# Optimization experiments

Hardware: AMD Instinct MI355X
Metric: run time of the kernel (lower is better)

Reference implementation:

```python
import jax, jax.numpy as jnp
import numpy as np

N_EMBD = 1024
N_HEAD = 16
B, T = 8, 1024
EPS = 1e-5


def setup_inputs() -> dict:
    key = jax.random.key(0)
    ks = jax.random.split(key, 12)
    C = N_EMBD
    s_in = 1.0 / np.sqrt(C)
    s_ff = 1.0 / np.sqrt(4 * C)
    inp = {
        "x": jax.random.normal(ks[0], (B, T, C), dtype=jnp.float32),
        "mask": jnp.tril(jnp.ones((T, T), dtype=jnp.int32))[None, None, :, :],
        "ln1_w": jnp.ones((C,), jnp.float32),
        "ln1_b": jnp.zeros((C,), jnp.float32),
        "ln2_w": jnp.ones((C,), jnp.float32),
        "ln2_b": jnp.zeros((C,), jnp.float32),
        "wq": jax.random.normal(ks[1], (C, C), jnp.float32) * s_in,
        "bq": jnp.zeros((C,), jnp.float32),
        "wk": jax.random.normal(ks[2], (C, C), jnp.float32) * s_in,
        "bk": jnp.zeros((C,), jnp.float32),
        "wv": jax.random.normal(ks[3], (C, C), jnp.float32) * s_in,
        "bv": jnp.zeros((C,), jnp.float32),
        "wo": jax.random.normal(ks[4], (C, C), jnp.float32) * s_in,
        "bo": jnp.zeros((C,), jnp.float32),
        "w1": jax.random.normal(ks[5], (C, 4 * C), jnp.float32) * s_in,
        "b1": jnp.zeros((4 * C,), jnp.float32),
        "w2": jax.random.normal(ks[6], (4 * C, C), jnp.float32) * s_ff,
        "b2": jnp.zeros((C,), jnp.float32),
    }
    return inp


def _layer_norm(x, w, b):
    mu = jnp.mean(x, axis=-1, keepdims=True)
    var = jnp.mean(jnp.square(x - mu), axis=-1, keepdims=True)
    return (x - mu) * jax.lax.rsqrt(var + EPS) * w + b


def reference(x, mask, ln1_w, ln1_b, ln2_w, ln2_b,
              wq, bq, wk, bk, wv, bv, wo, bo, w1, b1, w2, b2):
    Bx, Tx, C = x.shape
    H = N_HEAD
    d = C // H
    h = _layer_norm(x, ln1_w, ln1_b)
    q = (h @ wq + bq).reshape(Bx, Tx, H, d)
    k = (h @ wk + bk).reshape(Bx, Tx, H, d)
    v = (h @ wv + bv).reshape(Bx, Tx, H, d)
    # [B,H,Tq,Tk] scores, scaled by sqrt(head_dim)
    scores = jnp.einsum('bqhd,bkhd->bhqk', q, k) / jnp.sqrt(jnp.float32(d))
    scores = jnp.where(mask == 0, -jnp.inf, scores)
    attn = jax.nn.softmax(scores, axis=-1)
    ctx = jnp.einsum('bhqk,bkhd->bqhd', attn, v).reshape(Bx, Tx, C)
    x = x + (ctx @ wo + bo)
    h2 = _layer_norm(x, ln2_w, ln2_b)
    ff = jax.nn.gelu(h2 @ w1 + b1, approximate=False) @ w2 + b2
    return x + ff
```

## Files before the change

### kernel.cpp

```cpp
#include <hip/hip_runtime.h>
#include <hip/hip_bf16.h>
#include <math.h>


#define DEVI __device__ __forceinline__

typedef __attribute__((ext_vector_type(4))) float floatx4;
typedef __attribute__((ext_vector_type(16))) float floatx16;
typedef __attribute__((ext_vector_type(8))) short shortx8;

DEVI ushort f2b(float f) {
    __hip_bfloat16 h = __float2bfloat16(f);
    return __builtin_bit_cast(ushort, h);
}

DEVI void gl_lds16(const ushort* g, ushort* l) {
    __builtin_amdgcn_global_load_lds(
        (const __attribute__((address_space(1))) void*)g,
        (__attribute__((address_space(3))) void*)l, 16, 0, 0);
}

DEVI float gelu_f(float v) {
    const float u0 = 0.7978845608f * v * (1.0f + 0.044715f * v * v);
    const float u  = fminf(fmaxf(u0, -15.0f), 15.0f);
    const float e  = exp2f(u * 2.885390082f);
    const float th = 1.0f - 2.0f / (e + 1.0f);
    return 0.5f * v * (1.0f + th);
}

__global__ void transp4_kernel(const float* __restrict__ s0, const float* __restrict__ s1,
                               const float* __restrict__ s2, const float* __restrict__ s3,
                               ushort* __restrict__ d0, ushort* __restrict__ d1,
                               ushort* __restrict__ d2, ushort* __restrict__ d3) {
    const int z = blockIdx.z;
    const float* src = (z == 0) ? s0 : (z == 1) ? s1 : (z == 2) ? s2 : s3;
    ushort*      dst = (z == 0) ? d0 : (z == 1) ? d1 : (z == 2) ? d2 : d3;
    __shared__ float tile[32][33];
    const int c0 = blockIdx.x * 32, r0 = blockIdx.y * 32;
    const int tx = threadIdx.x, ty = threadIdx.y;
#pragma unroll
    for (int i = 0; i < 32; i += 8)
        tile[ty + i][tx] = src[(size_t)(r0 + ty + i) * 1024 + c0 + tx];
    __syncthreads();
#pragma unroll
    for (int i = 0; i < 32; i += 8)
        dst[(size_t)(c0 + ty + i) * 1024 + r0 + tx] = f2b(tile[tx][ty + i]);
}

__global__ void transp_kernel(const float* __restrict__ src,
                              ushort* __restrict__ dst, int R, int C) {
    __shared__ float tile[32][33];
    const int c0 = blockIdx.x * 32, r0 = blockIdx.y * 32;
    const int tx = threadIdx.x, ty = threadIdx.y;
#pragma unroll
    for (int i = 0; i < 32; i += 8)
        tile[ty + i][tx] = src[(size_t)(r0 + ty + i) * C + c0 + tx];
    __syncthreads();
#pragma unroll
    for (int i = 0; i < 32; i += 8)
        dst[(size_t)(c0 + ty + i) * R + r0 + tx] = f2b(tile[tx][ty + i]);
}

__global__ __launch_bounds__(256)
void ln_kernel(const float* __restrict__ x, const float* __restrict__ w,
               const float* __restrict__ b, ushort* __restrict__ out) {
    __shared__ float red[8];
    const int m = blockIdx.x;
    const int tid = threadIdx.x;
    const float4 xv = *(const float4*)&x[(size_t)m * 1024 + tid * 4];
    float s  = xv.x + xv.y + xv.z + xv.w;
    float s2 = xv.x * xv.x + xv.y * xv.y + xv.z * xv.z + xv.w * xv.w;
#pragma unroll
    for (int o = 32; o >= 1; o >>= 1) {
        s  += __shfl_xor(s, o, 64);
        s2 += __shfl_xor(s2, o, 64);
    }
    const int wv_ = tid >> 6;
    if ((tid & 63) == 0) { red[wv_] = s; red[4 + wv_] = s2; }
    __syncthreads();
    s  = red[0] + red[1] + red[2] + red[3];
    s2 = red[4] + red[5] + red[6] + red[7];
    const float mu   = s * (1.0f / 1024.0f);
    const float var  = s2 * (1.0f / 1024.0f) - mu * mu;
    const float rstd = rsqrtf(var + 1e-5f);
    const float4 wv = *(const float4*)&w[tid * 4];
    const float4 bv = *(const float4*)&b[tid * 4];
    ushort o4[4];
    o4[0] = f2b((xv.x - mu) * rstd * wv.x + bv.x);
    o4[1] = f2b((xv.y - mu) * rstd * wv.y + bv.y);
    o4[2] = f2b((xv.z - mu) * rstd * wv.z + bv.z);
    o4[3] = f2b((xv.w - mu) * rstd * wv.w + bv.w);
    *(uint2*)&out[(size_t)m * 1024 + tid * 4] = *(uint2*)o4;
}

template <int MODE>
__global__ __launch_bounds__(256, 2)
void gemm_big(const ushort* __restrict__ A, const ushort* __restrict__ Bt,
              const float* __restrict__ biasQ, const float* __restrict__ biasK,
              const float* __restrict__ biasV,
              void* __restrict__ out, void* __restrict__ out2, void* __restrict__ out3,
              int N, int K) {
    __shared__ ushort lds[(256 + 128) * 64];
    ushort* sA = lds;
    ushort* sB = lds + 256 * 64;

    const int tid  = threadIdx.x;
    const int lane = tid & 63;
    const int wave = tid >> 6;
    const int l31  = lane & 31;
    const int half = lane >> 5;
    const int wm   = (wave & 1) * 128;
    const int wn   = (wave >> 1) * 64;
    const int m0   = blockIdx.y * 256;
    const int n0   = blockIdx.x * 128;

    floatx16 acc[4][2] = {};

    const int lrow = lane >> 3;
    const int scb  = (lane & 7) ^ lrow;
    const ushort* Ag = A  + (size_t)(m0 + wave * 8 + lrow) * K + scb * 8;
    const ushort* Bg = Bt + (size_t)(n0 + wave * 8 + lrow) * K + scb * 8;

    for (int k0 = 0; k0 < K; k0 += 64) {
        __syncthreads();
#pragma unroll
        for (int p = 0; p < 8; ++p)
            gl_lds16(Ag + (size_t)(p * 32) * K + k0, sA + (p * 32 + wave * 8) * 64);
#pragma unroll
        for (int p = 0; p < 4; ++p)
            gl_lds16(Bg + (size_t)(p * 32) * K + k0, sB + (p * 32 + wave * 8) * 64);
        __syncthreads();
#pragma unroll
        for (int ks = 0; ks < 4; ++ks) {
            const int cx = ks * 2 + half;
            shortx8 af[4], bf[2];
#pragma unroll
            for (int i = 0; i < 4; ++i) {
                const int r = wm + i * 32 + l31;
                af[i] = *(const shortx8*)&sA[r * 64 + (cx ^ (r & 7)) * 8];
            }
#pragma unroll
            for (int j = 0; j < 2; ++j) {
                const int r = wn + j * 32 + l31;
                bf[j] = *(const shortx8*)&sB[r * 64 + (cx ^ (r & 7)) * 8];
            }
#pragma unroll
            for (int i = 0; i < 4; ++i)
#pragma unroll
                for (int j = 0; j < 2; ++j)
                    acc[i][j] = __builtin_amdgcn_mfma_f32_32x32x16_bf16(
                        af[i], bf[j], acc[i][j], 0, 0, 0);
        }
    }

    if constexpr (MODE == 1) {
        const int mat = n0 >> 10;
        if (mat < 2) {
            const float* bp = (mat == 0) ? biasQ : biasK;
            ushort* dst = (mat == 0) ? (ushort*)out : (ushort*)out2;
            const int bb = m0 >> 10;
            const int tbase = m0 & 1023;
#pragma unroll
            for (int i = 0; i < 4; ++i)
#pragma unroll
                for (int j = 0; j < 2; ++j) {
                    const int cn = (n0 & 1023) + wn + j * 32 + l31;
                    const float bv = bp[cn];
                    const int h = cn >> 6, dd = cn & 63;
#pragma unroll
                    for (int reg = 0; reg < 16; ++reg) {
                        const int t = tbase + wm + i * 32 + (reg & 3) + 8 * (reg >> 2) + 4 * half;
                        dst[((size_t)(bb * 16 + h) * 1024 + t) * 64 + dd] =
                            f2b(acc[i][j][reg] + bv);
                    }
                }
        } else {
            ushort* T = lds;
            const int vb = n0 - 2048;
            const int bb = m0 >> 10;
#pragma unroll
            for (int hf = 0; hf < 2; ++hf) {
                __syncthreads();
                if ((wave & 1) == hf) {
#pragma unroll
                    for (int i = 0; i < 4; ++i)
#pragma unroll
                        for (int j = 0; j < 2; ++j) {
                            const int dim = wn + j * 32 + l31;
                            const float bv = biasV[vb + dim];
#pragma unroll
                            for (int rq = 0; rq < 4; ++rq) {
                                const int tloc = i * 32 + 8 * rq + 4 * half;
                                ushort pk[4];
#pragma unroll
                                for (int e = 0; e < 4; ++e)
                                    pk[e] = f2b(acc[i][j][rq * 4 + e] + bv);
                                *(uint2*)&T[dim * 136 + tloc] = *(uint2*)pk;
                            }
                        }
                }
                __syncthreads();
#pragma unroll
                for (int pass = 0; pass < 8; ++pass) {
                    const int row = pass * 16 + (tid >> 4);
                    const int cb  = (tid & 15) * 8;
                    const uint4 val = *(const uint4*)&T[row * 136 + cb];
                    const int dd = vb + row;
                    const int h = dd >> 6, dl = dd & 63;
                    const int t = (m0 & 1023) + hf * 128 + cb;
                    *(uint4*)&((ushort*)out3)[((size_t)(bb * 16 + h) * 64 + dl) * 1024 + t] = val;
                }
            }
        }
    } else {
#pragma unroll
        for (int i = 0; i < 4; ++i)
#pragma unroll
            for (int j = 0; j < 2; ++j) {
                const int gn = n0 + wn + j * 32 + l31;
                const float bv = biasQ[gn];
#pragma unroll
                for (int reg = 0; reg < 16; ++reg) {
                    const int gm = m0 + wm + i * 32 + (reg & 3) + 8 * (reg >> 2) + 4 * half;
                    const float v = acc[i][j][reg] + bv;
                    ((ushort*)out)[(size_t)gm * N + gn] = f2b(gelu_f(v));
                }
            }
    }
}

__global__ __launch_bounds__(256)
void gemm_res(const ushort* __restrict__ A, const ushort* __restrict__ Bt,
              const float* __restrict__ bias, float* __restrict__ out,
              const float* __restrict__ resid, int N, int K) {
    __shared__ ushort lds[128 * 64 * 2];
    ushort* sA = lds;
    ushort* sB = lds + 128 * 64;

    const int tid  = threadIdx.x;
    const int lane = tid & 63;
    const int wave = tid >> 6;
    const int l31  = lane & 31;
    const int half = lane >> 5;
    const int wm   = (wave & 1) * 64;
    const int wn   = (wave >> 1) * 64;
    const int m0   = blockIdx.y * 128;
    const int n0   = blockIdx.x * 128;

    floatx16 acc[2][2] = {};

    const int lrow = lane >> 3;
    const int scb  = (lane & 7) ^ lrow;
    const ushort* Ag = A  + (size_t)(m0 + wave * 8 + lrow) * K + scb * 8;
    const ushort* Bg = Bt + (size_t)(n0 + wave * 8 + lrow) * K + scb * 8;

    for (int k0 = 0; k0 < K; k0 += 64) {
        __syncthreads();
#pragma unroll
        for (int p = 0; p < 4; ++p) {
            gl_lds16(Ag + (size_t)(p * 32) * K + k0, sA + (p * 32 + wave * 8) * 64);
            gl_lds16(Bg + (size_t)(p * 32) * K + k0, sB + (p * 32 + wave * 8) * 64);
        }
        __syncthreads();
#pragma unroll
        for (int ks = 0; ks < 4; ++ks) {
            const int cx = ks * 2 + half;
            shortx8 af[2], bf[2];
#pragma unroll
            for (int i = 0; i < 2; ++i) {
                const int r = wm + i * 32 + l31;
                af[i] = *(const shortx8*)&sA[r * 64 + (cx ^ (r & 7)) * 8];
            }
#pragma unroll
            for (int j = 0; j < 2; ++j) {
                const int r = wn + j * 32 + l31;
                bf[j] = *(const shortx8*)&sB[r * 64 + (cx ^ (r & 7)) * 8];
            }
#pragma unroll
            for (int i = 0; i < 2; ++i)
#pragma unroll
                for (int j = 0; j < 2; ++j)
                    acc[i][j] = __builtin_amdgcn_mfma_f32_32x32x16_bf16(
                        af[i], bf[j], acc[i][j], 0, 0, 0);
        }
    }
#pragma unroll
    for (int i = 0; i < 2; ++i)
#pragma unroll
        for (int j = 0; j < 2; ++j) {
            const int gn = n0 + wn + j * 32 + l31;
            const float bv = bias[gn];
#pragma unroll
            for (int reg = 0; reg < 16; ++reg) {
                const int gm = m0 + wm + i * 32 + (reg & 3) + 8 * (reg >> 2) + 4 * half;
                out[(size_t)gm * N + gn] =
                    acc[i][j][reg] + bv + resid[(size_t)gm * N + gn];
            }
        }
}

__global__ __launch_bounds__(256)
void attn_kernel(const ushort* __restrict__ Q, const ushort* __restrict__ Kk,
                 const ushort* __restrict__ Vt, ushort* __restrict__ ctx) {
    __shared__ ushort sK[64 * 64];
    __shared__ ushort sV[64 * 64];
    __shared__ ushort sP[4][16 * 72];

    const int tid  = threadIdx.x;
    const int lane = tid & 63;
    const int wave = tid >> 6;
    const int quad = lane >> 4;
    const int l15  = lane & 15;

    const int qb = 15 - (blockIdx.x >> 7);
    const int bh = blockIdx.x & 127;
    const size_t base = (size_t)bh << 16;
    const int bb = bh >> 4, h = bh & 15;

    const int lrow = lane >> 3;
    const int scb  = (lane & 7) ^ lrow;
    const ushort* Kg = Kk + base + (size_t)(wave * 8 + lrow) * 64 + scb * 8;
    const ushort* Vg = Vt + base + (size_t)(wave * 8 + lrow) * 1024 + scb * 8;

    const int qrow = qb * 64 + wave * 16 + l15;
    const shortx8 qf0 = *(const shortx8*)&Q[base + (size_t)qrow * 64 + quad * 8];
    const shortx8 qf1 = *(const shortx8*)&Q[base + (size_t)qrow * 64 + 32 + quad * 8];

    const float SC = 0.125f * 1.44269504f;

    float mstate[4], lstate[4];
    floatx4 oacc[4] = {};
#pragma unroll
    for (int r = 0; r < 4; ++r) { mstate[r] = -__builtin_inff(); lstate[r] = 0.0f; }

    for (int kt = 0; kt <= qb; ++kt) {
        __syncthreads();
#pragma unroll
        for (int p = 0; p < 2; ++p) {
            gl_lds16(Kg + (size_t)kt * 4096 + (size_t)p * 2048,
                     sK + (p * 32 + wave * 8) * 64);
            gl_lds16(Vg + (size_t)kt * 64 + (size_t)p * 32 * 1024,
                     sV + (p * 32 + wave * 8) * 64);
        }
        __syncthreads();

        floatx4 s[4];
#pragma unroll
        for (int nt = 0; nt < 4; ++nt) {
            const int r = nt * 16 + l15;
            const int c0 = quad ^ (r & 7);
            const int c1 = (4 + quad) ^ (r & 7);
            const shortx8 kf0 = *(const shortx8*)&sK[r * 64 + c0 * 8];
            const shortx8 kf1 = *(const shortx8*)&sK[r * 64 + c1 * 8];
            floatx4 z = {};
            z = __builtin_amdgcn_mfma_f32_16x16x32_bf16(qf0, kf0, z, 0, 0, 0);
            z = __builtin_amdgcn_mfma_f32_16x16x32_bf16(qf1, kf1, z, 0, 0, 0);
            s[nt] = z;
        }
#pragma unroll
        for (int nt = 0; nt < 4; ++nt)
#pragma unroll
            for (int r = 0; r < 4; ++r) {
                float sv = s[nt][r] * SC;
                if (kt == qb) {
                    const int col = nt * 16 + l15;
                    const int row = wave * 16 + quad * 4 + r;
                    if (col > row) sv = -__builtin_inff();
                }
                s[nt][r] = sv;
            }
        float mnew[4], alpha[4];
#pragma unroll
        for (int r = 0; r < 4; ++r) {
            float mt = fmaxf(fmaxf(s[0][r], s[1][r]), fmaxf(s[2][r], s[3][r]));
#pragma unroll
            for (int o = 8; o >= 1; o >>= 1) mt = fmaxf(mt, __shfl_xor(mt, o, 64));
            mnew[r]  = fmaxf(mstate[r], mt);
            alpha[r] = exp2f(mstate[r] - mnew[r]);
            mstate[r] = mnew[r];
        }
#pragma unroll
        for (int r = 0; r < 4; ++r) {
            float rs = 0.0f;
#pragma unroll
            for (int nt = 0; nt < 4; ++nt) {
                const float p = exp2f(s[nt][r] - mnew[r]);
                s[nt][r] = p;
                rs += p;
            }
#pragma unroll
            for (int o = 8; o >= 1; o >>= 1) rs += __shfl_xor(rs, o, 64);
            lstate[r] = alpha[r] * lstate[r] + rs;
#pragma unroll
            for (int dt = 0; dt < 4; ++dt) oacc[dt][r] *= alpha[r];
        }
#pragma unroll
        for (int nt = 0; nt < 4; ++nt)
#pragma unroll
            for (int r = 0; r < 4; ++r)
                sP[wave][(quad * 4 + r) * 72 + nt * 16 + l15] = f2b(s[nt][r]);
        __asm__ volatile("s_waitcnt lgkmcnt(0)" ::: "memory");
        const shortx8 pf0 = *(const shortx8*)&sP[wave][l15 * 72 + quad * 8];
        const shortx8 pf1 = *(const shortx8*)&sP[wave][l15 * 72 + 32 + quad * 8];
#pragma unroll
        for (int dt = 0; dt < 4; ++dt) {
            const int r = dt * 16 + l15;
            const int c0 = quad ^ (r & 7);
            const int c1 = (4 + quad) ^ (r & 7);
            const shortx8 v0 = *(const shortx8*)&sV[r * 64 + c0 * 8];
            const shortx8 v1 = *(const shortx8*)&sV[r * 64 + c1 * 8];
            oacc[dt] = __builtin_amdgcn_mfma_f32_16x16x32_bf16(pf0, v0, oacc[dt], 0, 0, 0);
            oacc[dt] = __builtin_amdgcn_mfma_f32_16x16x32_bf16(pf1, v1, oacc[dt], 0, 0, 0);
        }
    }
#pragma unroll
    for (int dt = 0; dt < 4; ++dt)
#pragma unroll
        for (int r = 0; r < 4; ++r) {
            const int t = qb * 64 + wave * 16 + quad * 4 + r;
            const int dim = dt * 16 + l15;
            const float v = oacc[dt][r] / lstate[r];
            ctx[(size_t)(bb * 1024 + t) * 1024 + h * 64 + dim] = f2b(v);
        }
}

extern "C" void kernel_launch(void* const* d_in, const int* in_sizes, int n_in,
                              void* d_out, int out_size, void* d_ws, size_t ws_size,
                              hipStream_t stream) {
    const float* x    = (const float*)d_in[0];
    const float* ln1w = (const float*)d_in[2];
    const float* ln1b = (const float*)d_in[3];
    const float* ln2w = (const float*)d_in[4];
    const float* ln2b = (const float*)d_in[5];
    const float* wq   = (const float*)d_in[6];
    const float* bq   = (const float*)d_in[7];
    const float* wk   = (const float*)d_in[8];
    const float* bk   = (const float*)d_in[9];
    const float* wv   = (const float*)d_in[10];
    const float* bv   = (const float*)d_in[11];
    const float* wo   = (const float*)d_in[12];
    const float* bo   = (const float*)d_in[13];
    const float* w1   = (const float*)d_in[14];
    const float* b1   = (const float*)d_in[15];
    const float* w2   = (const float*)d_in[16];
    const float* b2   = (const float*)d_in[17];

    char* ws = (char*)d_ws;
    const size_t MB = 1024 * 1024;
    ushort* WQKVT = (ushort*)(ws + 0 * MB);
    ushort* WOT   = (ushort*)(ws + 6 * MB);
    ushort* W1T   = (ushort*)(ws + 8 * MB);
    ushort* W2T   = (ushort*)(ws + 16 * MB);
    ushort* H1    = (ushort*)(ws + 24 * MB);
    ushort* H2    = H1;
    ushort* Qb    = (ushort*)(ws + 40 * MB);
    ushort* Kb    = (ushort*)(ws + 56 * MB);
    ushort* Vbt   = (ushort*)(ws + 72 * MB);
    ushort* FF1   = (ushort*)(ws + 40 * MB);
    ushort* CTX   = (ushort*)(ws + 104 * MB);

    float* xout = (float*)d_out;

    const dim3 tb(32, 8);
    transp4_kernel<<<dim3(32, 32, 4), tb, 0, stream>>>(
        wq, wk, wv, wo,
        WQKVT, WQKVT + 1024 * 1024, WQKVT + 2048 * 1024, WOT);
    transp_kernel<<<dim3(128, 32), tb, 0, stream>>>(w1, W1T, 1024, 4096);
    transp_kernel<<<dim3(32, 128), tb, 0, stream>>>(w2, W2T, 4096, 1024);

    ln_kernel<<<8192, 256, 0, stream>>>(x, ln1w, ln1b, H1);

    gemm_big<1><<<dim3(24, 32), 256, 0, stream>>>(H1, WQKVT, bq, bk, bv,
                                                  Qb, Kb, Vbt, 3072, 1024);

    attn_kernel<<<2048, 256, 0, stream>>>(Qb, Kb, Vbt, CTX);

    gemm_res<<<dim3(8, 64), 256, 0, stream>>>(CTX, WOT, bo, xout, x, 1024, 1024);

    ln_kernel<<<8192, 256, 0, stream>>>(xout, ln2w, ln2b, H2);

    gemm_big<3><<<dim3(32, 32), 256, 0, stream>>>(H2, W1T, b1, nullptr, nullptr,
                                                  FF1, nullptr, nullptr, 4096, 1024);

    gemm_res<<<dim3(8, 64), 256, 0, stream>>>(FF1, W2T, b2, xout, xout, 1024, 4096);

    (void)in_sizes; (void)n_in; (void)out_size; (void)ws_size;
}
```

Baseline: 497.4 us.

## Replace gemm_big with 8-wave 256x256 double-buffered pipelined GEMM

Replaces the 4-wave 256x128 GEMM used for the QKV projection and FF1 with an 8-wave 256x256 tile kernel. It double-buffers LDS, issues global-to-LDS loads for the next k-tiles interleaved with four MFMA phases, and raises MFMA priority with s_setprio. It also switches to 16x16x32 MFMAs and remaps workgroups for L2 locality. The intent is to hide global load latency and raise MFMA utilisation. The cost is 128KB of LDS per block, which limits occupancy, plus more complex manual waitcnt and barrier scheduling.

```diff
diff --git a/kernel.cpp b/kernel.cpp
--- a/kernel.cpp
+++ b/kernel.cpp
@@ -93,139 +93,207 @@
     *(uint2*)&out[(size_t)m * 1024 + tid * 4] = *(uint2*)o4;
 }
 
+
+#define STAGE_A(j, h) { const int c_ = (j) & 1;                                         \
+    gl_lds16(pA + (size_t)((h) * 128) * K + (j) * 64,                                   \
+             lds + c_ * 16384 + (h) * 8192 + dOff);                                     \
+    gl_lds16(pA + (size_t)((h) * 128 + 8) * K + (j) * 64,                               \
+             lds + c_ * 16384 + (h) * 8192 + dOff + 512); }
+
+#define STAGE_B(j, h) { const int c_ = (j) & 1;                                         \
+    gl_lds16(pB + (size_t)((h) * 128) * K + (j) * 64,                                   \
+             lds + 32768 + c_ * 16384 + (h) * 8192 + dOff);                             \
+    gl_lds16(pB + (size_t)((h) * 128 + 8) * K + (j) * 64,                               \
+             lds + 32768 + c_ * 16384 + (h) * 8192 + dOff + 512); }
+
+#define LOAD_A(mq, c) { const ushort* ap = lds + (c) * 16384 + (mq) * 8192;             \
+    _Pragma("unroll") for (int mi = 0; mi < 4; ++mi) {                                  \
+        af[mi][0] = *(const shortx8*)&ap[aBase + mi * 1024];                            \
+        af[mi][1] = *(const shortx8*)&ap[(aBase ^ 32) + mi * 1024]; } }
+
+#define LOAD_B(nq, c) { const ushort* bp = lds + 32768 + (c) * 16384 + (nq) * 8192;     \
+    _Pragma("unroll") for (int ni = 0; ni < 2; ++ni) {                                  \
+        bf[ni][0] = *(const shortx8*)&bp[bBase + ni * 1024];                            \
+        bf[ni][1] = *(const shortx8*)&bp[(bBase ^ 32) + ni * 1024]; } }
+
+#define MFMA16(mq, nq) {                                                                \
+    _Pragma("unroll") for (int mi = 0; mi < 4; ++mi)                                    \
+    _Pragma("unroll") for (int ni = 0; ni < 2; ++ni)                                    \
+    _Pragma("unroll") for (int ks = 0; ks < 2; ++ks)                                    \
+        acc[mq][mi][nq][ni] = __builtin_amdgcn_mfma_f32_16x16x32_bf16(                  \
+            af[mi][ks], bf[ni][ks], acc[mq][mi][nq][ni], 0, 0, 0); }
+
+#define PH_SYNC() { __builtin_amdgcn_s_barrier();                                       \
+    asm volatile("s_waitcnt lgkmcnt(0)" ::: "memory");                                  \
+    __builtin_amdgcn_sched_barrier(0); }
+
 template <int MODE>
-__global__ __launch_bounds__(256, 2)
-void gemm_big(const ushort* __restrict__ A, const ushort* __restrict__ Bt,
-              const float* __restrict__ biasQ, const float* __restrict__ biasK,
-              const float* __restrict__ biasV,
-              void* __restrict__ out, void* __restrict__ out2, void* __restrict__ out3,
-              int N, int K) {
-    __shared__ ushort lds[(256 + 128) * 64];
-    ushort* sA = lds;
-    ushort* sB = lds + 256 * 64;
+__global__ __launch_bounds__(512, 2)
+void gemm8(const ushort* __restrict__ A, const ushort* __restrict__ Bt,
+           const float* __restrict__ biasQ, const float* __restrict__ biasK,
+           const float* __restrict__ biasV,
+           void* __restrict__ out, void* __restrict__ out2, void* __restrict__ out3,
+           int N, int K) {
+    __shared__ __align__(16) ushort lds[65536];
 
     const int tid  = threadIdx.x;
     const int lane = tid & 63;
-    const int wave = tid >> 6;
-    const int l31  = lane & 31;
-    const int half = lane >> 5;
-    const int wm   = (wave & 1) * 128;
-    const int wn   = (wave >> 1) * 64;
-    const int m0   = blockIdx.y * 256;
-    const int n0   = blockIdx.x * 128;
-
-    floatx16 acc[4][2] = {};
-
-    const int lrow = lane >> 3;
-    const int scb  = (lane & 7) ^ lrow;
-    const ushort* Ag = A  + (size_t)(m0 + wave * 8 + lrow) * K + scb * 8;
-    const ushort* Bg = Bt + (size_t)(n0 + wave * 8 + lrow) * K + scb * 8;
-
-    for (int k0 = 0; k0 < K; k0 += 64) {
-        __syncthreads();
-#pragma unroll
-        for (int p = 0; p < 8; ++p)
-            gl_lds16(Ag + (size_t)(p * 32) * K + k0, sA + (p * 32 + wave * 8) * 64);
-#pragma unroll
-        for (int p = 0; p < 4; ++p)
-            gl_lds16(Bg + (size_t)(p * 32) * K + k0, sB + (p * 32 + wave * 8) * 64);
-        __syncthreads();
-#pragma unroll
-        for (int ks = 0; ks < 4; ++ks) {
-            const int cx = ks * 2 + half;
-            shortx8 af[4], bf[2];
-#pragma unroll
-            for (int i = 0; i < 4; ++i) {
-                const int r = wm + i * 32 + l31;
-                af[i] = *(const shortx8*)&sA[r * 64 + (cx ^ (r & 7)) * 8];
-            }
-#pragma unroll
-            for (int j = 0; j < 2; ++j) {
-                const int r = wn + j * 32 + l31;
-                bf[j] = *(const shortx8*)&sB[r * 64 + (cx ^ (r & 7)) * 8];
-            }
-#pragma unroll
-            for (int i = 0; i < 4; ++i)
-#pragma unroll
-                for (int j = 0; j < 2; ++j)
-                    acc[i][j] = __builtin_amdgcn_mfma_f32_32x32x16_bf16(
-                        af[i], bf[j], acc[i][j], 0, 0, 0);
+    const int w    = tid >> 6;
+    const int wr   = w >> 2;
+    const int wc   = w & 3;
+
+    int bx = blockIdx.x, by = blockIdx.y;
+    {
+        const int nwg = gridDim.x * gridDim.y;
+        if ((nwg & 7) == 0) {
+            const int flat = by * gridDim.x + bx;
+            const int cpx  = nwg >> 3;
+            const int wg   = (flat & 7) * cpx + (flat >> 3);
+            bx = wg % gridDim.x;
+            by = wg / gridDim.x;
+        }
+    }
+    const int m0 = by * 256;
+    const int n0 = bx * 256;
+    const int NT = K >> 6;
+
+    floatx4 acc[2][4][2][2] = {};
+
+    const int lr3 = lane >> 3;
+    const int sc  = (lane & 7) ^ lr3;
+    const ushort* pA = A  + (size_t)(m0 + w * 16 + lr3) * K + sc * 8;
+    const ushort* pB = Bt + (size_t)(n0 + w * 16 + lr3) * K + sc * 8;
+    const int dOff = w * 1024;
+
+    const int c0    = (lane >> 4) ^ (lane & 7);
+    const int aBase = (wr * 64 + (lane & 15)) * 64 + c0 * 8;
+    const int bBase = (wc * 32 + (lane & 15)) * 64 + c0 * 8;
+
+    shortx8 af[4][2], bf[2][2];
+
+    STAGE_A(0, 0); STAGE_B(0, 1); STAGE_A(0, 1); STAGE_B(0, 0);
+    STAGE_A(1, 0); STAGE_B(1, 1);
+
+#pragma unroll 1
+    for (int j = 0; j < NT; ++j) {
+        const int c = j & 1;
+        if (j == NT - 1) { asm volatile("s_waitcnt vmcnt(0)" ::: "memory"); }
+        else             { asm volatile("s_waitcnt vmcnt(4)" ::: "memory"); }
+        __builtin_amdgcn_s_barrier();
+
+        LOAD_A(0, c); LOAD_B(0, c);
+        if (j + 1 < NT) STAGE_A(j + 1, 1);
+        PH_SYNC();
+        __builtin_amdgcn_s_setprio(1); MFMA16(0, 0); __builtin_amdgcn_s_setprio(0);
+        __builtin_amdgcn_s_barrier();
+
+        LOAD_B(1, c);
+        if (j + 1 < NT) STAGE_B(j + 1, 0);
+        PH_SYNC();
+        __builtin_amdgcn_s_setprio(1); MFMA16(0, 1); __builtin_amdgcn_s_setprio(0);
+        __builtin_amdgcn_s_barrier();
+
+        LOAD_A(1, c);
+        if (j + 2 < NT) STAGE_A(j + 2, 0);
+        PH_SYNC();
+        __builtin_amdgcn_s_setprio(1); MFMA16(1, 1); __builtin_amdgcn_s_setprio(0);
+        __builtin_amdgcn_s_barrier();
+
+        LOAD_B(0, c);
+        if (j + 2 < NT) STAGE_B(j + 2, 1);
+        PH_SYNC();
+        __builtin_amdgcn_s_setprio(1); MFMA16(1, 0); __builtin_amdgcn_s_setprio(0);
+    }
+
+    if constexpr (MODE == 3) {
+        float bvals[2][2];
+#pragma unroll
+        for (int nq = 0; nq < 2; ++nq)
+#pragma unroll
+            for (int ni = 0; ni < 2; ++ni)
+                bvals[nq][ni] = biasQ[n0 + nq * 128 + wc * 32 + ni * 16 + (lane & 15)];
+        ushort* o = (ushort*)out;
+#pragma unroll
+        for (int mq = 0; mq < 2; ++mq)
+#pragma unroll
+        for (int mi = 0; mi < 4; ++mi)
+#pragma unroll
+        for (int nq = 0; nq < 2; ++nq)
+#pragma unroll
+        for (int ni = 0; ni < 2; ++ni) {
+            const int gm0 = m0 + mq * 128 + wr * 64 + mi * 16 + (lane >> 4) * 4;
+            const int gn  = n0 + nq * 128 + wc * 32 + ni * 16 + (lane & 15);
+#pragma unroll
+            for (int r = 0; r < 4; ++r)
+                o[(size_t)(gm0 + r) * N + gn] =
+                    f2b(gelu_f(acc[mq][mi][nq][ni][r] + bvals[nq][ni]));
         }
     }
 
     if constexpr (MODE == 1) {
-        const int mat = n0 >> 10;
+        const int mat   = n0 >> 10;
+        const int bb    = m0 >> 10;
+        const int tbase = m0 & 1023;
         if (mat < 2) {
             const float* bp = (mat == 0) ? biasQ : biasK;
             ushort* dst = (mat == 0) ? (ushort*)out : (ushort*)out2;
-            const int bb = m0 >> 10;
-            const int tbase = m0 & 1023;
-#pragma unroll
-            for (int i = 0; i < 4; ++i)
-#pragma unroll
-                for (int j = 0; j < 2; ++j) {
-                    const int cn = (n0 & 1023) + wn + j * 32 + l31;
-                    const float bv = bp[cn];
-                    const int h = cn >> 6, dd = cn & 63;
-#pragma unroll
-                    for (int reg = 0; reg < 16; ++reg) {
-                        const int t = tbase + wm + i * 32 + (reg & 3) + 8 * (reg >> 2) + 4 * half;
-                        dst[((size_t)(bb * 16 + h) * 1024 + t) * 64 + dd] =
-                            f2b(acc[i][j][reg] + bv);
+            float bvals[2][2];
+#pragma unroll
+            for (int nq = 0; nq < 2; ++nq)
+#pragma unroll
+                for (int ni = 0; ni < 2; ++ni)
+                    bvals[nq][ni] =
+                        bp[(n0 & 1023) + nq * 128 + wc * 32 + ni * 16 + (lane & 15)];
+#pragma unroll
+            for (int mq = 0; mq < 2; ++mq)
+#pragma unroll
+            for (int mi = 0; mi < 4; ++mi)
+#pragma unroll
+            for (int nq = 0; nq < 2; ++nq)
+#pragma unroll
+            for (int ni = 0; ni < 2; ++ni) {
+                const int cn = (n0 & 1023) + nq * 128 + wc * 32 + ni * 16 + (lane & 15);
+                const int h = cn >> 6, dd = cn & 63;
+                const int t0 = tbase + mq * 128 + wr * 64 + mi * 16 + (lane >> 4) * 4;
+#pragma unroll
+                for (int r = 0; r < 4; ++r)
+                    dst[((size_t)(bb * 16 + h) * 1024 + t0 + r) * 64 + dd] =
+                        f2b(acc[mq][mi][nq][ni][r] + bvals[nq][ni]);
+            }
+        } else {
+            const int vb = n0 - 2048;
+            ushort* T = lds;
+            ushort* Vt = (ushort*)out3;
+            const int dimL = wc * 32 + (lane & 15);
+#pragma unroll 1
+            for (int dh = 0; dh < 2; ++dh) {
+                __syncthreads();
+#pragma unroll
+                for (int ni = 0; ni < 2; ++ni) {
+                    const float bv = biasV[vb + dh * 128 + dimL + ni * 16];
+#pragma unroll
+                    for (int mq = 0; mq < 2; ++mq)
+#pragma unroll
+                    for (int mi = 0; mi < 4; ++mi) {
+                        const int t0 = mq * 128 + wr * 64 + mi * 16 + (lane >> 4) * 4;
+#pragma unroll
+                        for (int r = 0; r < 4; ++r)
+                            T[(dimL + ni * 16) * 264 + t0 + r] =
+                                f2b(acc[mq][mi][dh][ni][r] + bv);
                     }
                 }
-        } else {
-            ushort* T = lds;
-            const int vb = n0 - 2048;
-            const int bb = m0 >> 10;
-#pragma unroll
-            for (int hf = 0; hf < 2; ++hf) {
                 __syncthreads();
-                if ((wave & 1) == hf) {
-#pragma unroll
-                    for (int i = 0; i < 4; ++i)
-#pragma unroll
-                        for (int j = 0; j < 2; ++j) {
-                            const int dim = wn + j * 32 + l31;
-                            const float bv = biasV[vb + dim];
-#pragma unroll
-                            for (int rq = 0; rq < 4; ++rq) {
-                                const int tloc = i * 32 + 8 * rq + 4 * half;
-                                ushort pk[4];
-#pragma unroll
-                                for (int e = 0; e < 4; ++e)
-                                    pk[e] = f2b(acc[i][j][rq * 4 + e] + bv);
-                                *(uint2*)&T[dim * 136 + tloc] = *(uint2*)pk;
-                            }
-                        }
+#pragma unroll
+                for (int it = 0; it < 8; ++it) {
+                    const int idx = it * 512 + tid;
+                    const int row = idx >> 5, ch = idx & 31;
+                    const uint4 vv = *(const uint4*)&T[row * 264 + ch * 8];
+                    const int d  = vb + dh * 128 + row;
+                    const int hh = d >> 6, dl = d & 63;
+                    *(uint4*)&Vt[((size_t)(bb * 16 + hh) * 64 + dl) * 1024 + tbase + ch * 8] = vv;
                 }
-                __syncthreads();
-#pragma unroll
-                for (int pass = 0; pass < 8; ++pass) {
-                    const int row = pass * 16 + (tid >> 4);
-                    const int cb  = (tid & 15) * 8;
-                    const uint4 val = *(const uint4*)&T[row * 136 + cb];
-                    const int dd = vb + row;
-                    const int h = dd >> 6, dl = dd & 63;
-                    const int t = (m0 & 1023) + hf * 128 + cb;
-                    *(uint4*)&((ushort*)out3)[((size_t)(bb * 16 + h) * 64 + dl) * 1024 + t] = val;
-                }
-            }
-        }
-    } else {
-#pragma unroll
-        for (int i = 0; i < 4; ++i)
-#pragma unroll
-            for (int j = 0; j < 2; ++j) {
-                const int gn = n0 + wn + j * 32 + l31;
-                const float bv = biasQ[gn];
-#pragma unroll
-                for (int reg = 0; reg < 16; ++reg) {
-                    const int gm = m0 + wm + i * 32 + (reg & 3) + 8 * (reg >> 2) + 4 * half;
-                    const float v = acc[i][j][reg] + bv;
-                    ((ushort*)out)[(size_t)gm * N + gn] = f2b(gelu_f(v));
-                }
-            }
+            }
+        }
     }
 }
 
@@ -470,8 +538,8 @@
 
     ln_kernel<<<8192, 256, 0, stream>>>(x, ln1w, ln1b, H1);
 
-    gemm_big<1><<<dim3(24, 32), 256, 0, stream>>>(H1, WQKVT, bq, bk, bv,
-                                                  Qb, Kb, Vbt, 3072, 1024);
+    gemm8<1><<<dim3(12, 32), 512, 0, stream>>>(H1, WQKVT, bq, bk, bv,
+                                               Qb, Kb, Vbt, 3072, 1024);
 
     attn_kernel<<<2048, 256, 0, stream>>>(Qb, Kb, Vbt, CTX);
 
@@ -479,8 +547,8 @@
 
     ln_kernel<<<8192, 256, 0, stream>>>(xout, ln2w, ln2b, H2);
 
-    gemm_big<3><<<dim3(32, 32), 256, 0, stream>>>(H2, W1T, b1, nullptr, nullptr,
-                                                  FF1, nullptr, nullptr, 4096, 1024);
+    gemm8<3><<<dim3(16, 32), 512, 0, stream>>>(H2, W1T, b1, nullptr, nullptr,
+                                               FF1, nullptr, nullptr, 4096, 1024);
 
     gemm_res<<<dim3(8, 64), 256, 0, stream>>>(FF1, W2T, b2, xout, xout, 1024, 4096);
 
```

Result: slower. 572.4 us (+15.1%).

## Unify GEMMs into one 128x128 16x16-MFMA kernel with LDS-staged epilogues

Applied to the files above, without the earlier changes.

Replaces the 256x128 and 128x128 GEMM kernels with one templated 128x128-tile kernel using 16x16x32 bf16 MFMA, launch bounds allowing 4 blocks per CU, and XCD-aware block remapping for L2 locality. Every epilogue (QKV head scatter, GELU, residual add) now goes through LDS staging so global writes are 16-byte coalesced instead of scattered 2-byte or 4-byte stores. The cost is smaller tiles, which means more global and LDS traffic per FLOP for the large GEMMs, plus extra barriers in the epilogue.

```diff
diff --git a/kernel.cpp b/kernel.cpp
--- a/kernel.cpp
+++ b/kernel.cpp
@@ -6,7 +6,6 @@
 #define DEVI __device__ __forceinline__
 
 typedef __attribute__((ext_vector_type(4))) float floatx4;
-typedef __attribute__((ext_vector_type(16))) float floatx16;
 typedef __attribute__((ext_vector_type(8))) short shortx8;
 
 DEVI ushort f2b(float f) {
@@ -94,209 +93,213 @@
 }
 
 template <int MODE>
-__global__ __launch_bounds__(256, 2)
-void gemm_big(const ushort* __restrict__ A, const ushort* __restrict__ Bt,
-              const float* __restrict__ biasQ, const float* __restrict__ biasK,
-              const float* __restrict__ biasV,
-              void* __restrict__ out, void* __restrict__ out2, void* __restrict__ out3,
-              int N, int K) {
-    __shared__ ushort lds[(256 + 128) * 64];
-    ushort* sA = lds;
-    ushort* sB = lds + 256 * 64;
+__global__ __launch_bounds__(256, 4)
+void gemm97(const ushort* __restrict__ A, const ushort* __restrict__ Bt,
+            const float* __restrict__ biasQ, const float* __restrict__ biasK,
+            const float* __restrict__ biasV,
+            void* __restrict__ out, void* __restrict__ out2, void* __restrict__ out3,
+            const float* __restrict__ resid, int N, int K) {
+    __shared__ __align__(128) ushort lds[18432];
 
     const int tid  = threadIdx.x;
     const int lane = tid & 63;
-    const int wave = tid >> 6;
-    const int l31  = lane & 31;
-    const int half = lane >> 5;
-    const int wm   = (wave & 1) * 128;
-    const int wn   = (wave >> 1) * 64;
-    const int m0   = blockIdx.y * 256;
-    const int n0   = blockIdx.x * 128;
-
-    floatx16 acc[4][2] = {};
-
-    const int lrow = lane >> 3;
-    const int scb  = (lane & 7) ^ lrow;
-    const ushort* Ag = A  + (size_t)(m0 + wave * 8 + lrow) * K + scb * 8;
-    const ushort* Bg = Bt + (size_t)(n0 + wave * 8 + lrow) * K + scb * 8;
+    const int w    = tid >> 6;
+    const int wr   = w >> 1;
+    const int wc   = w & 1;
+
+    int bx = blockIdx.x, by = blockIdx.y;
+    {
+        const int nwg = gridDim.x * gridDim.y;
+        if ((nwg & 7) == 0) {
+            const int flat = by * gridDim.x + bx;
+            const int cpx  = nwg >> 3;
+            const int wg   = (flat & 7) * cpx + (flat >> 3);
+            bx = wg % gridDim.x;
+            by = wg / gridDim.x;
+        }
+    }
+    const int m0 = by * 128;
+    const int n0 = bx * 128;
+
+    floatx4 acc[4][4] = {};
+
+    const int lr3 = lane >> 3;
+    const int sc  = (lane & 7) ^ lr3;
+    const ushort* pA = A  + (size_t)(m0 + w * 32 + lr3) * K + sc * 8;
+    const ushort* pB = Bt + (size_t)(n0 + w * 32 + lr3) * K + sc * 8;
+    ushort* sAd = lds + w * 2048;
+    ushort* sBd = lds + 8192 + w * 2048;
+    const size_t k8 = (size_t)8 * K, k16 = (size_t)16 * K, k24 = (size_t)24 * K;
+
+    const int c0f = (lane >> 4) ^ (lane & 7);
+    const int aIdx = (wr * 64 + (lane & 15)) * 64 + c0f * 8;
+    const int bIdx = (wc * 64 + (lane & 15)) * 64 + c0f * 8;
+    const ushort* ar0 = lds + aIdx;
+    const ushort* ar1 = lds + (aIdx ^ 32);
+    const ushort* br0 = lds + 8192 + bIdx;
+    const ushort* br1 = lds + 8192 + (bIdx ^ 32);
 
     for (int k0 = 0; k0 < K; k0 += 64) {
         __syncthreads();
-#pragma unroll
-        for (int p = 0; p < 8; ++p)
-            gl_lds16(Ag + (size_t)(p * 32) * K + k0, sA + (p * 32 + wave * 8) * 64);
-#pragma unroll
-        for (int p = 0; p < 4; ++p)
-            gl_lds16(Bg + (size_t)(p * 32) * K + k0, sB + (p * 32 + wave * 8) * 64);
+        gl_lds16(pA + k0,       sAd);
+        gl_lds16(pA + k8  + k0, sAd + 512);
+        gl_lds16(pA + k16 + k0, sAd + 1024);
+        gl_lds16(pA + k24 + k0, sAd + 1536);
+        gl_lds16(pB + k0,       sBd);
+        gl_lds16(pB + k8  + k0, sBd + 512);
+        gl_lds16(pB + k16 + k0, sBd + 1024);
+        gl_lds16(pB + k24 + k0, sBd + 1536);
+        asm volatile("s_waitcnt vmcnt(0)" ::: "memory");
         __syncthreads();
-#pragma unroll
-        for (int ks = 0; ks < 4; ++ks) {
-            const int cx = ks * 2 + half;
-            shortx8 af[4], bf[2];
-#pragma unroll
-            for (int i = 0; i < 4; ++i) {
-                const int r = wm + i * 32 + l31;
-                af[i] = *(const shortx8*)&sA[r * 64 + (cx ^ (r & 7)) * 8];
-            }
-#pragma unroll
-            for (int j = 0; j < 2; ++j) {
-                const int r = wn + j * 32 + l31;
-                bf[j] = *(const shortx8*)&sB[r * 64 + (cx ^ (r & 7)) * 8];
-            }
-#pragma unroll
-            for (int i = 0; i < 4; ++i)
-#pragma unroll
-                for (int j = 0; j < 2; ++j)
-                    acc[i][j] = __builtin_amdgcn_mfma_f32_32x32x16_bf16(
-                        af[i], bf[j], acc[i][j], 0, 0, 0);
+
+        shortx8 af[4][2], bf[4][2];
+#pragma unroll
+        for (int mi = 0; mi < 4; ++mi) {
+            af[mi][0] = *(const shortx8*)&ar0[mi * 1024];
+            af[mi][1] = *(const shortx8*)&ar1[mi * 1024];
+        }
+#pragma unroll
+        for (int ni = 0; ni < 4; ++ni) {
+            bf[ni][0] = *(const shortx8*)&br0[ni * 1024];
+            bf[ni][1] = *(const shortx8*)&br1[ni * 1024];
+        }
+#pragma unroll
+        for (int mi = 0; mi < 4; ++mi)
+#pragma unroll
+            for (int ni = 0; ni < 4; ++ni) {
+                acc[mi][ni] = __builtin_amdgcn_mfma_f32_16x16x32_bf16(
+                    af[mi][0], bf[ni][0], acc[mi][ni], 0, 0, 0);
+                acc[mi][ni] = __builtin_amdgcn_mfma_f32_16x16x32_bf16(
+                    af[mi][1], bf[ni][1], acc[mi][ni], 0, 0, 0);
+            }
+    }
+    __syncthreads();
+
+    const int colL  = wc * 64 + (lane & 15);
+    const int rbase = wr * 64 + ((lane >> 4) << 2);
+
+    if constexpr (MODE == 3) {
+        float bvals[4];
+#pragma unroll
+        for (int ni = 0; ni < 4; ++ni) bvals[ni] = biasQ[n0 + colL + ni * 16];
+        ushort* T = lds;
+#pragma unroll
+        for (int mi = 0; mi < 4; ++mi)
+#pragma unroll
+        for (int ni = 0; ni < 4; ++ni) {
+            const int t0 = rbase + mi * 16;
+#pragma unroll
+            for (int r = 0; r < 4; ++r)
+                T[(t0 + r) * 136 + colL + ni * 16] =
+                    f2b(gelu_f(acc[mi][ni][r] + bvals[ni]));
+        }
+        __syncthreads();
+        ushort* o = (ushort*)out;
+#pragma unroll
+        for (int it = 0; it < 8; ++it) {
+            const int idx = it * 256 + tid;
+            const int row = idx >> 4, ch = idx & 15;
+            const uint4 vv = *(const uint4*)&T[row * 136 + ch * 8];
+            *(uint4*)&o[(size_t)(m0 + row) * N + n0 + ch * 8] = vv;
+        }
+    }
+
+    if constexpr (MODE == 2) {
+        float bvals[4];
+#pragma unroll
+        for (int ni = 0; ni < 4; ++ni) bvals[ni] = biasQ[n0 + colL + ni * 16];
+        float* T = (float*)lds;
+        float* o = (float*)out;
+#pragma unroll
+        for (int half = 0; half < 2; ++half) {
+            if (wr == half) {
+#pragma unroll
+                for (int mi = 0; mi < 4; ++mi)
+#pragma unroll
+                for (int ni = 0; ni < 4; ++ni) {
+                    const int t0 = mi * 16 + ((lane >> 4) << 2);
+#pragma unroll
+                    for (int r = 0; r < 4; ++r)
+                        T[(t0 + r) * 132 + colL + ni * 16] =
+                            acc[mi][ni][r] + bvals[ni];
+                }
+            }
+            __syncthreads();
+#pragma unroll
+            for (int it = 0; it < 8; ++it) {
+                const int idx = it * 256 + tid;
+                const int row = idx >> 5, ch = idx & 31;
+                float4 tv = *(const float4*)&T[row * 132 + ch * 4];
+                const size_t go = (size_t)(m0 + half * 64 + row) * N + n0 + ch * 4;
+                const float4 rv = *(const float4*)&resid[go];
+                tv.x += rv.x; tv.y += rv.y; tv.z += rv.z; tv.w += rv.w;
+                *(float4*)&o[go] = tv;
+            }
+            __syncthreads();
         }
     }
 
     if constexpr (MODE == 1) {
-        const int mat = n0 >> 10;
+        const int mat   = n0 >> 10;
+        const int bb    = m0 >> 10;
+        const int tbase = m0 & 1023;
         if (mat < 2) {
             const float* bp = (mat == 0) ? biasQ : biasK;
             ushort* dst = (mat == 0) ? (ushort*)out : (ushort*)out2;
-            const int bb = m0 >> 10;
-            const int tbase = m0 & 1023;
-#pragma unroll
-            for (int i = 0; i < 4; ++i)
-#pragma unroll
-                for (int j = 0; j < 2; ++j) {
-                    const int cn = (n0 & 1023) + wn + j * 32 + l31;
-                    const float bv = bp[cn];
-                    const int h = cn >> 6, dd = cn & 63;
-#pragma unroll
-                    for (int reg = 0; reg < 16; ++reg) {
-                        const int t = tbase + wm + i * 32 + (reg & 3) + 8 * (reg >> 2) + 4 * half;
-                        dst[((size_t)(bb * 16 + h) * 1024 + t) * 64 + dd] =
-                            f2b(acc[i][j][reg] + bv);
-                    }
+            float bvals[4];
+#pragma unroll
+            for (int ni = 0; ni < 4; ++ni)
+                bvals[ni] = bp[(n0 & 1023) + colL + ni * 16];
+            ushort* T = lds;
+#pragma unroll
+            for (int mi = 0; mi < 4; ++mi)
+#pragma unroll
+            for (int ni = 0; ni < 4; ++ni) {
+                const int t0 = rbase + mi * 16;
+#pragma unroll
+                for (int r = 0; r < 4; ++r)
+                    T[(t0 + r) * 136 + colL + ni * 16] =
+                        f2b(acc[mi][ni][r] + bvals[ni]);
+            }
+            __syncthreads();
+#pragma unroll
+            for (int it = 0; it < 8; ++it) {
+                const int idx = it * 256 + tid;
+                const int row = idx >> 4, ch = idx & 15;
+                const uint4 vv = *(const uint4*)&T[row * 136 + ch * 8];
+                const int cg = (n0 & 1023) + ch * 8;
+                const int h = cg >> 6, dd = cg & 63;
+                const int t = tbase + row;
+                *(uint4*)&dst[((size_t)(bb * 16 + h) * 1024 + t) * 64 + dd] = vv;
+            }
+        } else {
+            const int vb = n0 - 2048;
+            ushort* T = lds;
+            ushort* Vt = (ushort*)out3;
+#pragma unroll
+            for (int ni = 0; ni < 4; ++ni) {
+                const float bv = biasV[vb + colL + ni * 16];
+#pragma unroll
+                for (int mi = 0; mi < 4; ++mi) {
+                    const int t0 = rbase + mi * 16;
+#pragma unroll
+                    for (int r = 0; r < 4; ++r)
+                        T[(colL + ni * 16) * 136 + t0 + r] =
+                            f2b(acc[mi][ni][r] + bv);
                 }
-        } else {
-            ushort* T = lds;
-            const int vb = n0 - 2048;
-            const int bb = m0 >> 10;
-#pragma unroll
-            for (int hf = 0; hf < 2; ++hf) {
-                __syncthreads();
-                if ((wave & 1) == hf) {
-#pragma unroll
-                    for (int i = 0; i < 4; ++i)
-#pragma unroll
-                        for (int j = 0; j < 2; ++j) {
-                            const int dim = wn + j * 32 + l31;
-                            const float bv = biasV[vb + dim];
-#pragma unroll
-                            for (int rq = 0; rq < 4; ++rq) {
-                                const int tloc = i * 32 + 8 * rq + 4 * half;
-                                ushort pk[4];
-#pragma unroll
-                                for (int e = 0; e < 4; ++e)
-                                    pk[e] = f2b(acc[i][j][rq * 4 + e] + bv);
-                                *(uint2*)&T[dim * 136 + tloc] = *(uint2*)pk;
-                            }
-                        }
-                }
-                __syncthreads();
-#pragma unroll
-                for (int pass = 0; pass < 8; ++pass) {
-                    const int row = pass * 16 + (tid >> 4);
-                    const int cb  = (tid & 15) * 8;
-                    const uint4 val = *(const uint4*)&T[row * 136 + cb];
-                    const int dd = vb + row;
-                    const int h = dd >> 6, dl = dd & 63;
-                    const int t = (m0 & 1023) + hf * 128 + cb;
-                    *(uint4*)&((ushort*)out3)[((size_t)(bb * 16 + h) * 64 + dl) * 1024 + t] = val;
-                }
-            }
-        }
-    } else {
-#pragma unroll
-        for (int i = 0; i < 4; ++i)
-#pragma unroll
-            for (int j = 0; j < 2; ++j) {
-                const int gn = n0 + wn + j * 32 + l31;
-                const float bv = biasQ[gn];
-#pragma unroll
-                for (int reg = 0; reg < 16; ++reg) {
-                    const int gm = m0 + wm + i * 32 + (reg & 3) + 8 * (reg >> 2) + 4 * half;
-                    const float v = acc[i][j][reg] + bv;
-                    ((ushort*)out)[(size_t)gm * N + gn] = f2b(gelu_f(v));
-                }
-            }
-    }
-}
-
-__global__ __launch_bounds__(256)
-void gemm_res(const ushort* __restrict__ A, const ushort* __restrict__ Bt,
-              const float* __restrict__ bias, float* __restrict__ out,
-              const float* __restrict__ resid, int N, int K) {
-    __shared__ ushort lds[128 * 64 * 2];
-    ushort* sA = lds;
-    ushort* sB = lds + 128 * 64;
-
-    const int tid  = threadIdx.x;
-    const int lane = tid & 63;
-    const int wave = tid >> 6;
-    const int l31  = lane & 31;
-    const int half = lane >> 5;
-    const int wm   = (wave & 1) * 64;
-    const int wn   = (wave >> 1) * 64;
-    const int m0   = blockIdx.y * 128;
-    const int n0   = blockIdx.x * 128;
-
-    floatx16 acc[2][2] = {};
-
-    const int lrow = lane >> 3;
-    const int scb  = (lane & 7) ^ lrow;
-    const ushort* Ag = A  + (size_t)(m0 + wave * 8 + lrow) * K + scb * 8;
-    const ushort* Bg = Bt + (size_t)(n0 + wave * 8 + lrow) * K + scb * 8;
-
-    for (int k0 = 0; k0 < K; k0 += 64) {
-        __syncthreads();
-#pragma unroll
-        for (int p = 0; p < 4; ++p) {
-            gl_lds16(Ag + (size_t)(p * 32) * K + k0, sA + (p * 32 + wave * 8) * 64);
-            gl_lds16(Bg + (size_t)(p * 32) * K + k0, sB + (p * 32 + wave * 8) * 64);
-        }
-        __syncthreads();
-#pragma unroll
-        for (int ks = 0; ks < 4; ++ks) {
-            const int cx = ks * 2 + half;
-            shortx8 af[2], bf[2];
-#pragma unroll
-            for (int i = 0; i < 2; ++i) {
-                const int r = wm + i * 32 + l31;
-                af[i] = *(const shortx8*)&sA[r * 64 + (cx ^ (r & 7)) * 8];
-            }
-#pragma unroll
-            for (int j = 0; j < 2; ++j) {
-                const int r = wn + j * 32 + l31;
-                bf[j] = *(const shortx8*)&sB[r * 64 + (cx ^ (r & 7)) * 8];
-            }
-#pragma unroll
-            for (int i = 0; i < 2; ++i)
-#pragma unroll
-                for (int j = 0; j < 2; ++j)
-                    acc[i][j] = __builtin_amdgcn_mfma_f32_32x32x16_bf16(
-                        af[i], bf[j], acc[i][j], 0, 0, 0);
-        }
-    }
-#pragma unroll
-    for (int i = 0; i < 2; ++i)
-#pragma unroll
-        for (int j = 0; j < 2; ++j) {
-            const int gn = n0 + wn + j * 32 + l31;
-            const float bv = bias[gn];
-#pragma unroll
-            for (int reg = 0; reg < 16; ++reg) {
-                const int gm = m0 + wm + i * 32 + (reg & 3) + 8 * (reg >> 2) + 4 * half;
-                out[(size_t)gm * N + gn] =
-                    acc[i][j][reg] + bv + resid[(size_t)gm * N + gn];
-            }
-        }
+            }
+            __syncthreads();
+#pragma unroll
+            for (int it = 0; it < 8; ++it) {
+                const int idx = it * 256 + tid;
+                const int dim = idx >> 4, ch = idx & 15;
+                const uint4 vv = *(const uint4*)&T[dim * 136 + ch * 8];
+                const int d  = vb + dim;
+                const int hh = d >> 6, dl = d & 63;
+                *(uint4*)&Vt[((size_t)(bb * 16 + hh) * 64 + dl) * 1024 + tbase + ch * 8] = vv;
+            }
+        }
+    }
 }
 
 __global__ __launch_bounds__(256)
@@ -470,19 +473,21 @@
 
     ln_kernel<<<8192, 256, 0, stream>>>(x, ln1w, ln1b, H1);
 
-    gemm_big<1><<<dim3(24, 32), 256, 0, stream>>>(H1, WQKVT, bq, bk, bv,
-                                                  Qb, Kb, Vbt, 3072, 1024);
+    gemm97<1><<<dim3(24, 64), 256, 0, stream>>>(H1, WQKVT, bq, bk, bv,
+                                                Qb, Kb, Vbt, nullptr, 3072, 1024);
 
     attn_kernel<<<2048, 256, 0, stream>>>(Qb, Kb, Vbt, CTX);
 
-    gemm_res<<<dim3(8, 64), 256, 0, stream>>>(CTX, WOT, bo, xout, x, 1024, 1024);
+    gemm97<2><<<dim3(8, 64), 256, 0, stream>>>(CTX, WOT, bo, nullptr, nullptr,
+                                               xout, nullptr, nullptr, x, 1024, 1024);
 
     ln_kernel<<<8192, 256, 0, stream>>>(xout, ln2w, ln2b, H2);
 
-    gemm_big<3><<<dim3(32, 32), 256, 0, stream>>>(H2, W1T, b1, nullptr, nullptr,
-                                                  FF1, nullptr, nullptr, 4096, 1024);
-
-    gemm_res<<<dim3(8, 64), 256, 0, stream>>>(FF1, W2T, b2, xout, xout, 1024, 4096);
+    gemm97<3><<<dim3(32, 64), 256, 0, stream>>>(H2, W1T, b1, nullptr, nullptr,
+                                                FF1, nullptr, nullptr, nullptr, 4096, 1024);
+
+    gemm97<2><<<dim3(8, 64), 256, 0, stream>>>(FF1, W2T, b2, nullptr, nullptr,
+                                               xout, nullptr, nullptr, xout, 1024, 4096);
 
     (void)in_sizes; (void)n_in; (void)out_size; (void)ws_size;
 }
```

New measurement: 499.6 us. No clear change (+0.4%).
